# Optimization experiments

Hardware: AMD Instinct MI355X
Metric: run time of the kernel (lower is better)

The kernel has to match this reference:

```python
import jax, jax.numpy as jnp
import numpy as np

N_NODES = 100000
N_EDGES = 1600000
NODE_DIM = 128
EDGE_DIM = 32
HIDDEN = 64
OUT = 64


def setup_inputs() -> dict:
    key = jax.random.key(0)
    ks = jax.random.split(key, 16)
    s = lambda d: 1.0 / np.sqrt(d)
    inp = {
        'node_features': jax.random.normal(ks[0], (N_NODES, NODE_DIM), dtype=jnp.float32),
        'edge_indices': jax.random.randint(ks[1], (2, N_EDGES), 0, N_NODES, dtype=jnp.int64),
        'edge_features': jax.random.normal(ks[2], (N_EDGES, EDGE_DIM), dtype=jnp.float32),
        # node_transform / edge_transform
        'wn': jax.random.uniform(ks[3], (NODE_DIM, HIDDEN), jnp.float32, -s(NODE_DIM), s(NODE_DIM)),
        'bn': jax.random.uniform(ks[4], (HIDDEN,), jnp.float32, -s(NODE_DIM), s(NODE_DIM)),
        'we': jax.random.uniform(ks[5], (EDGE_DIM, HIDDEN), jnp.float32, -s(EDGE_DIM), s(EDGE_DIM)),
        'be': jax.random.uniform(ks[6], (HIDDEN,), jnp.float32, -s(EDGE_DIM), s(EDGE_DIM)),
        # message_mlp: Linear(2H,H) -> ReLU -> Linear(H,OUT)
        'wm1': jax.random.uniform(ks[7], (2 * HIDDEN, HIDDEN), jnp.float32, -s(2 * HIDDEN), s(2 * HIDDEN)),
        'bm1': jax.random.uniform(ks[8], (HIDDEN,), jnp.float32, -s(2 * HIDDEN), s(2 * HIDDEN)),
        'wm2': jax.random.uniform(ks[9], (HIDDEN, OUT), jnp.float32, -s(HIDDEN), s(HIDDEN)),
        'bm2': jax.random.uniform(ks[10], (OUT,), jnp.float32, -s(HIDDEN), s(HIDDEN)),
        # update_mlp: Linear(NODE_DIM+OUT,H) -> ReLU -> Linear(H,OUT)
        'wu1': jax.random.uniform(ks[11], (NODE_DIM + OUT, HIDDEN), jnp.float32, -s(NODE_DIM + OUT), s(NODE_DIM + OUT)),
        'bu1': jax.random.uniform(ks[12], (HIDDEN,), jnp.float32, -s(NODE_DIM + OUT), s(NODE_DIM + OUT)),
        'wu2': jax.random.uniform(ks[13], (HIDDEN, OUT), jnp.float32, -s(HIDDEN), s(HIDDEN)),
        'bu2': jax.random.uniform(ks[14], (OUT,), jnp.float32, -s(HIDDEN), s(HIDDEN)),
    }
    return inp


def reference(node_features, edge_indices, edge_features, wn, bn, we, be,
              wm1, bm1, wm2, bm2, wu1, bu1, wu2, bu2):
    node_emb = node_features @ wn + bn              # [N, H]
    edge_emb = edge_features @ we + be              # [E, H]
    src, dst = edge_indices[0], edge_indices[1]
    messages = jnp.concatenate([node_emb[src], edge_emb], axis=-1)  # [E, 2H]
    messages = jax.nn.relu(messages @ wm1 + bm1) @ wm2 + bm2        # [E, OUT]
    aggregated = jax.ops.segment_sum(messages, dst, num_segments=node_emb.shape[0])  # [N, OUT]
    updated = jnp.concatenate([node_features, aggregated], axis=-1)  # [N, NODE_DIM+OUT]
    return jax.nn.relu(updated @ wu1 + bu1) @ wu2 + bu2              # [N, OUT]
```

## Files before the change

kernel.cpp:

```cpp
#include <hip/hip_runtime.h>

#define NN 100000
#define NE 1600000

typedef __attribute__((ext_vector_type(8))) short bf16x8;
typedef __attribute__((ext_vector_type(4))) float f32x4;

#define OFF_M    0
#define OFF_B    (OFF_M + 16384)
#define OFF_C    (OFF_B + 2048)
#define OFF_W2U  (OFF_C + 64)
#define OFF_D2   (OFF_W2U + 4096)
#define OFF_BFRG (OFF_D2 + 64)
#define OFF_MFRG (OFF_BFRG + 1024)
#define OFF_W2UF (OFF_MFRG + 8192)
#define OFF_WU2F (OFF_W2UF + 2048)
#define OFF_BSUM (OFF_WU2F + 2048)
#define OFF_BOFF (OFF_BSUM + 128)
#define OFF_PRA  (OFF_BOFF + 128)
#define OFF_PRAH (OFF_PRA + NN * 64)
#define OFF_PRU  (OFF_PRAH + NN * 32)
#define OFF_H    (OFF_PRU + NN * 64)
#define OFF_HIST (OFF_H + NN * 64)
#define OFF_STRT (OFF_HIST + NN)
#define OFF_POS  (OFF_STRT + NN + 4)
#define OFF_HS   (OFF_POS + NE)
#define WS_UNITS (OFF_HS + NE * 32)

__device__ __forceinline__ unsigned bfr(float x) {
  unsigned u = __float_as_uint(x);
  return (u + 0x7fffu + ((u >> 16) & 1u)) >> 16;
}
__device__ __forceinline__ float bf2f(unsigned short h) {
  return __uint_as_float(((unsigned)h) << 16);
}
__device__ __forceinline__ unsigned addrelu1(unsigned qa, unsigned pb) {
  float lo = __uint_as_float((qa & 0xffffu) << 16) +
             __uint_as_float((pb & 0xffffu) << 16);
  float hi = __uint_as_float(qa & 0xffff0000u) +
             __uint_as_float(pb & 0xffff0000u);
  lo = fmaxf(lo, 0.f);
  hi = fmaxf(hi, 0.f);
  return bfr(lo) | (bfr(hi) << 16);
}
__device__ __forceinline__ uint4 addrelu4(uint4 q, uint4 p) {
  return make_uint4(addrelu1(q.x, p.x), addrelu1(q.y, p.y),
                    addrelu1(q.z, p.z), addrelu1(q.w, p.w));
}

__global__ __launch_bounds__(256) void k_fold(
    const float* __restrict__ wn, const float* __restrict__ bn,
    const float* __restrict__ we, const float* __restrict__ be,
    const float* __restrict__ wm1, const float* __restrict__ bm1,
    const float* __restrict__ wm2, const float* __restrict__ bm2,
    const float* __restrict__ wu1, const float* __restrict__ wu2,
    float* __restrict__ M, float* __restrict__ B, float* __restrict__ c,
    float* __restrict__ W2U, float* __restrict__ d2,
    uint4* __restrict__ Bfrag, uint4* __restrict__ Mfrag,
    uint4* __restrict__ W2Uf, uint4* __restrict__ wu2f) {
  int t = blockIdx.x * 256 + threadIdx.x;
  if (t < 16384) {
    int k = t >> 7, j = t & 127;
    float acc;
    if (j < 64) {
      acc = 0.f;
      for (int h = 0; h < 64; ++h) acc += wn[k * 64 + h] * wm1[h * 64 + j];
    } else {
      acc = wu1[k * 64 + (j - 64)];
    }
    M[t] = acc;
  } else if (t < 16384 + 2048) {
    int u = t - 16384;
    int k = u >> 6, j = u & 63;
    float acc = 0.f;
    for (int h = 0; h < 64; ++h) acc += we[k * 64 + h] * wm1[(64 + h) * 64 + j];
    B[u] = acc;
  } else if (t < 16384 + 2048 + 64) {
    int j = t - (16384 + 2048);
    float acc = bm1[j];
    for (int h = 0; h < 64; ++h)
      acc += bn[h] * wm1[h * 64 + j] + be[h] * wm1[(64 + h) * 64 + j];
    c[j] = acc;
  } else if (t < 16384 + 2048 + 64 + 4096) {
    int u = t - (16384 + 2048 + 64);
    int k = u >> 6, j = u & 63;
    float acc = 0.f;
    for (int h = 0; h < 64; ++h) acc += wm2[k * 64 + h] * wu1[(128 + h) * 64 + j];
    W2U[u] = acc;
  } else if (t < 16384 + 2048 + 64 + 4096 + 64) {
    int j = t - (16384 + 2048 + 64 + 4096);
    float acc = 0.f;
    for (int h = 0; h < 64; ++h) acc += bm2[h] * wu1[(128 + h) * 64 + j];
    d2[j] = acc;
  } else if (t < 16384 + 2048 + 64 + 4096 + 64 + 256) {
    int u = t - (16384 + 2048 + 64 + 4096 + 64);
    int jb = u >> 6, l = u & 63;
    int g = l >> 4, n = l & 15;
    unsigned s[8];
#pragma unroll
    for (int i = 0; i < 8; ++i) {
      int k = g * 8 + i;
      int j = jb * 16 + n;
      float acc = 0.f;
      for (int h = 0; h < 64; ++h)
        acc += we[k * 64 + h] * wm1[(64 + h) * 64 + j];
      s[i] = bfr(acc);
    }
    Bfrag[jb * 64 + l] = make_uint4(s[0] | (s[1] << 16), s[2] | (s[3] << 16),
                                    s[4] | (s[5] << 16), s[6] | (s[7] << 16));
  } else if (t < 16384 + 2048 + 64 + 4096 + 64 + 256 + 2048) {
    int u = t - (16384 + 2048 + 64 + 4096 + 64 + 256);
    int jb = u >> 8, kb = (u >> 6) & 3, l = u & 63;
    int g = l >> 4, n = l & 15;
    int j = jb * 16 + n;
    unsigned s[8];
#pragma unroll
    for (int i = 0; i < 8; ++i) {
      int k = kb * 32 + g * 8 + i;
      float acc;
      if (j < 64) {
        acc = 0.f;
        for (int h = 0; h < 64; ++h) acc += wn[k * 64 + h] * wm1[h * 64 + j];
      } else {
        acc = wu1[k * 64 + (j - 64)];
      }
      s[i] = bfr(acc);
    }
    Mfrag[(jb * 4 + kb) * 64 + l] =
        make_uint4(s[0] | (s[1] << 16), s[2] | (s[3] << 16),
                   s[4] | (s[5] << 16), s[6] | (s[7] << 16));
  } else if (t < 16384 + 2048 + 64 + 4096 + 64 + 256 + 2048 + 512) {
    int u = t - (16384 + 2048 + 64 + 4096 + 64 + 256 + 2048);
    int jk = u >> 6, l = u & 63;
    int jb = jk >> 1, kb = jk & 1;
    int g = l >> 4, n = l & 15;
    int j = jb * 16 + n;
    unsigned s[8];
#pragma unroll
    for (int i = 0; i < 8; ++i) {
      int k = kb * 32 + g * 8 + i;
      float acc = 0.f;
      for (int h = 0; h < 64; ++h)
        acc += wm2[k * 64 + h] * wu1[(128 + h) * 64 + j];
      s[i] = bfr(acc);
    }
    W2Uf[jk * 64 + l] = make_uint4(s[0] | (s[1] << 16), s[2] | (s[3] << 16),
                                   s[4] | (s[5] << 16), s[6] | (s[7] << 16));
  } else if (t < 16384 + 2048 + 64 + 4096 + 64 + 256 + 2048 + 512 + 512) {
    int u = t - (16384 + 2048 + 64 + 4096 + 64 + 256 + 2048 + 512);
    int jk = u >> 6, l = u & 63;
    int jb = jk >> 1, kb = jk & 1;
    int g = l >> 4, n = l & 15;
    unsigned s[8];
#pragma unroll
    for (int i = 0; i < 8; ++i)
      s[i] = bfr(wu2[(size_t)(kb * 32 + g * 8 + i) * 64 + jb * 16 + n]);
    wu2f[jk * 64 + l] = make_uint4(s[0] | (s[1] << 16), s[2] | (s[3] << 16),
                                   s[4] | (s[5] << 16), s[6] | (s[7] << 16));
  }
}

__global__ __launch_bounds__(256) void k_node2(
    const float* __restrict__ nf, const uint4* __restrict__ Mfrag,
    float* __restrict__ PRA, uint4* __restrict__ PRAh,
    float* __restrict__ PRU, int writePRA) {
  __shared__ unsigned short ldsP[4][16 * 72];
  int wib = threadIdx.x >> 6;
  int lane = threadIdx.x & 63;
  int tile = blockIdx.x * 4 + wib;
  if (tile >= NN / 16) return;
  int m = lane & 15, g = lane >> 4;
  int node = tile * 16 + m;

  bf16x8 a[4];
#pragma unroll
  for (int kb = 0; kb < 4; ++kb) {
    const float* __restrict__ rp = &nf[(size_t)node * 128 + kb * 32 + g * 8];
    float4 f0 = *(const float4*)rp;
    float4 f1 = *(const float4*)(rp + 4);
    bf16x8 v;
    v[0] = (short)bfr(f0.x); v[1] = (short)bfr(f0.y);
    v[2] = (short)bfr(f0.z); v[3] = (short)bfr(f0.w);
    v[4] = (short)bfr(f1.x); v[5] = (short)bfr(f1.y);
    v[6] = (short)bfr(f1.z); v[7] = (short)bfr(f1.w);
    a[kb] = v;
  }

  const bf16x8* __restrict__ mfp = (const bf16x8*)Mfrag;
  unsigned short* __restrict__ lp = &ldsP[wib][0];
#pragma unroll
  for (int jb = 0; jb < 8; ++jb) {
    f32x4 acc = {0.f, 0.f, 0.f, 0.f};
    acc = __builtin_amdgcn_mfma_f32_16x16x32_bf16(a[0], mfp[(jb * 4 + 0) * 64 + lane], acc, 0, 0, 0);
    acc = __builtin_amdgcn_mfma_f32_16x16x32_bf16(a[1], mfp[(jb * 4 + 1) * 64 + lane], acc, 0, 0, 0);
    acc = __builtin_amdgcn_mfma_f32_16x16x32_bf16(a[2], mfp[(jb * 4 + 2) * 64 + lane], acc, 0, 0, 0);
    acc = __builtin_amdgcn_mfma_f32_16x16x32_bf16(a[3], mfp[(jb * 4 + 3) * 64 + lane], acc, 0, 0, 0);
    int col = (jb & 3) * 16 + m;
    if (jb < 4) {
#pragma unroll
      for (int r = 0; r < 4; ++r)
        lp[(g * 4 + r) * 72 + col] = (unsigned short)bfr(acc[r]);
      if (writePRA) {
#pragma unroll
        for (int r = 0; r < 4; ++r)
          PRA[(size_t)(tile * 16 + g * 4 + r) * 64 + col] = acc[r];
      }
    } else {
#pragma unroll
      for (int r = 0; r < 4; ++r)
        PRU[(size_t)(tile * 16 + g * 4 + r) * 64 + col] = acc[r];
    }
  }
  __syncthreads();

  int m2 = lane >> 2, lo = lane & 3;
  uint4 w0 = *(const uint4*)&ldsP[wib][m2 * 72 + lo * 8];
  uint4 w1 = *(const uint4*)&ldsP[wib][m2 * 72 + 32 + lo * 8];
  uint4* __restrict__ pp = &PRAh[(size_t)(tile * 16 + m2) * 8];
  pp[lo] = w0;
  pp[4 + lo] = w1;
}

__global__ __launch_bounds__(256) void k_hist(const int* __restrict__ idx,
                                              int* __restrict__ hist,
                                              int* __restrict__ posOf) {
  int e = blockIdx.x * 256 + threadIdx.x;
  if (e < NE) posOf[e] = atomicAdd(&hist[idx[NE + e]], 1);
}

__global__ __launch_bounds__(1024) void k_scanA(const int* __restrict__ hist,
                                                int* __restrict__ strt,
                                                int* __restrict__ bsum) {
  __shared__ int lds[1024];
  int t = threadIdx.x;
  int i = blockIdx.x * 1024 + t;
  int v = (i < NN) ? hist[i] : 0;
  lds[t] = v;
  __syncthreads();
  for (int off = 1; off < 1024; off <<= 1) {
    int u = (t >= off) ? lds[t - off] : 0;
    __syncthreads();
    lds[t] += u;
    __syncthreads();
  }
  if (i < NN) strt[i] = lds[t] - v;
  if (t == 1023) bsum[blockIdx.x] = lds[1023];
}

__global__ __launch_bounds__(128) void k_scanB(const int* __restrict__ bsum,
                                               int* __restrict__ boff,
                                               int* __restrict__ strt,
                                               int nblocks) {
  __shared__ int lds[128];
  int t = threadIdx.x;
  int v = (t < nblocks) ? bsum[t] : 0;
  lds[t] = v;
  __syncthreads();
  for (int off = 1; off < 128; off <<= 1) {
    int u = (t >= off) ? lds[t - off] : 0;
    __syncthreads();
    lds[t] += u;
    __syncthreads();
  }
  if (t < nblocks) boff[t] = lds[t] - v;
  if (t == 127) strt[NN] = lds[127];
}

__global__ __launch_bounds__(1024) void k_scanC(int* __restrict__ strt,
                                                const int* __restrict__ boff) {
  int i = blockIdx.x * 1024 + threadIdx.x;
  if (i < NN) strt[i] += boff[blockIdx.x];
}

__global__ __launch_bounds__(256) void k_msgh(
    const int* __restrict__ idx, const int* __restrict__ strt,
    const int* __restrict__ posOf, const float* __restrict__ ef,
    const uint4* __restrict__ Bfrag, const float* __restrict__ c,
    const uint4* __restrict__ PRAh, unsigned short* __restrict__ hS) {
  __shared__ unsigned short ldsQ[4][16 * 72];
  int wib = threadIdx.x >> 6;
  int lane = threadIdx.x & 63;
  int m = lane & 15, g = lane >> 4;
  int tile = blockIdx.x * 4 + wib;

  int m2 = lane >> 2, lo = lane & 3;
  int e6 = tile * 16 + m2;
  int src6 = idx[e6];
  int dst6 = idx[NE + e6];
  int pos6 = posOf[e6];
  uint4 p0 = PRAh[(size_t)src6 * 8 + lo];
  uint4 p1 = PRAh[(size_t)src6 * 8 + 4 + lo];
  int slot = strt[dst6] + pos6;

  const float* __restrict__ rp = &ef[(size_t)(tile * 16 + m) * 32 + g * 8];
  float4 f0 = *(const float4*)rp;
  float4 f1 = *(const float4*)(rp + 4);
  bf16x8 a;
  a[0] = (short)bfr(f0.x); a[1] = (short)bfr(f0.y);
  a[2] = (short)bfr(f0.z); a[3] = (short)bfr(f0.w);
  a[4] = (short)bfr(f1.x); a[5] = (short)bfr(f1.y);
  a[6] = (short)bfr(f1.z); a[7] = (short)bfr(f1.w);

  const bf16x8* __restrict__ bfp = (const bf16x8*)Bfrag;
  bf16x8 b0 = bfp[0 * 64 + lane];
  bf16x8 b1 = bfp[1 * 64 + lane];
  bf16x8 b2 = bfp[2 * 64 + lane];
  bf16x8 b3 = bfp[3 * 64 + lane];
  float cl0 = c[0 * 16 + m], cl1 = c[1 * 16 + m];
  float cl2 = c[2 * 16 + m], cl3 = c[3 * 16 + m];

  f32x4 z = {0.f, 0.f, 0.f, 0.f};
  f32x4 q0 = __builtin_amdgcn_mfma_f32_16x16x32_bf16(a, b0, z, 0, 0, 0);
  f32x4 q1 = __builtin_amdgcn_mfma_f32_16x16x32_bf16(a, b1, z, 0, 0, 0);
  f32x4 q2 = __builtin_amdgcn_mfma_f32_16x16x32_bf16(a, b2, z, 0, 0, 0);
  f32x4 q3 = __builtin_amdgcn_mfma_f32_16x16x32_bf16(a, b3, z, 0, 0, 0);

  unsigned short* __restrict__ lq = &ldsQ[wib][0];
#pragma unroll
  for (int r = 0; r < 4; ++r) {
    int mp = g * 4 + r;
    lq[mp * 72 + 0 * 16 + m] = (unsigned short)bfr(q0[r] + cl0);
    lq[mp * 72 + 1 * 16 + m] = (unsigned short)bfr(q1[r] + cl1);
    lq[mp * 72 + 2 * 16 + m] = (unsigned short)bfr(q2[r] + cl2);
    lq[mp * 72 + 3 * 16 + m] = (unsigned short)bfr(q3[r] + cl3);
  }
  __syncthreads();

  uint4 w0 = *(const uint4*)&ldsQ[wib][m2 * 72 + lo * 8];
  uint4 w1 = *(const uint4*)&ldsQ[wib][m2 * 72 + 32 + lo * 8];
  uint4 h0 = addrelu4(w0, p0);
  uint4 h1 = addrelu4(w1, p1);
  uint4* __restrict__ qp = (uint4*)(hS + (size_t)slot * 64);
  qp[lo] = h0;
  qp[4 + lo] = h1;
}

__global__ __launch_bounds__(256) void k_sum(
    const unsigned short* __restrict__ hS, const int* __restrict__ strt,
    unsigned* __restrict__ Hb) {
  int wib = threadIdx.x >> 6;
  int lane = threadIdx.x & 63;
  int n = blockIdx.x * 4 + wib;
  if (n >= NN) return;
  int s0 = strt[n], s1 = strt[n + 1];
  float acc = 0.f;
  int s = s0;
  for (; s + 4 <= s1; s += 4) {
    unsigned short a0 = hS[(size_t)(s + 0) * 64 + lane];
    unsigned short a1 = hS[(size_t)(s + 1) * 64 + lane];
    unsigned short a2 = hS[(size_t)(s + 2) * 64 + lane];
    unsigned short a3 = hS[(size_t)(s + 3) * 64 + lane];
    acc += (bf2f(a0) + bf2f(a1)) + (bf2f(a2) + bf2f(a3));
  }
  for (; s < s1; ++s) acc += bf2f(hS[(size_t)s * 64 + lane]);
  float other = __shfl_xor(acc, 1);
  if ((lane & 1) == 0)
    Hb[(size_t)n * 32 + (lane >> 1)] = bfr(acc) | (bfr(other) << 16);
}

__global__ __launch_bounds__(256) void k_update5(
    const unsigned* __restrict__ Hb, const int* __restrict__ strt,
    const float* __restrict__ PRU,
    const uint4* __restrict__ W2Uf, const float* __restrict__ d2,
    const float* __restrict__ bu1,
    const uint4* __restrict__ wu2f, const float* __restrict__ bu2,
    float* __restrict__ out) {
  __shared__ unsigned short ldsH[4][16 * 72];
  int wib = threadIdx.x >> 6;
  int lane = threadIdx.x & 63;
  int tile = blockIdx.x * 4 + wib;
  if (tile >= NN / 16) return;
  int m = lane & 15, g = lane >> 4;
  int node = tile * 16 + m;

  bf16x8 ah[2];
  ah[0] = *(const bf16x8*)&Hb[(size_t)node * 32 + 0 * 16 + g * 4];
  ah[1] = *(const bf16x8*)&Hb[(size_t)node * 32 + 1 * 16 + g * 4];

  float deg[4];
#pragma unroll
  for (int r = 0; r < 4; ++r) {
    int row = tile * 16 + g * 4 + r;
    deg[r] = (float)(strt[row + 1] - strt[row]);
  }

  const bf16x8* __restrict__ w2p = (const bf16x8*)W2Uf;
  const bf16x8* __restrict__ wup = (const bf16x8*)wu2f;
  unsigned short* __restrict__ lh = &ldsH[wib][0];

#pragma unroll
  for (int jb = 0; jb < 4; ++jb) {
    f32x4 acc = {0.f, 0.f, 0.f, 0.f};
    acc = __builtin_amdgcn_mfma_f32_16x16x32_bf16(ah[0], w2p[(jb * 2 + 0) * 64 + lane], acc, 0, 0, 0);
    acc = __builtin_amdgcn_mfma_f32_16x16x32_bf16(ah[1], w2p[(jb * 2 + 1) * 64 + lane], acc, 0, 0, 0);
    int col = jb * 16 + m;
    float dc = d2[col], bc = bu1[col];
#pragma unroll
    for (int r = 0; r < 4; ++r) {
      int row = tile * 16 + g * 4 + r;
      float pre = acc[r] + PRU[(size_t)row * 64 + col] + deg[r] * dc + bc;
      lh[(g * 4 + r) * 72 + col] = (unsigned short)bfr(fmaxf(pre, 0.f));
    }
  }
  __syncthreads();

  bf16x8 a2[2];
  a2[0] = *(const bf16x8*)&lh[m * 72 + 0 * 32 + g * 8];
  a2[1] = *(const bf16x8*)&lh[m * 72 + 1 * 32 + g * 8];
#pragma unroll
  for (int jb = 0; jb < 4; ++jb) {
    f32x4 acc = {0.f, 0.f, 0.f, 0.f};
    acc = __builtin_amdgcn_mfma_f32_16x16x32_bf16(a2[0], wup[(jb * 2 + 0) * 64 + lane], acc, 0, 0, 0);
    acc = __builtin_amdgcn_mfma_f32_16x16x32_bf16(a2[1], wup[(jb * 2 + 1) * 64 + lane], acc, 0, 0, 0);
    int col = jb * 16 + m;
    float bc = bu2[col];
#pragma unroll
    for (int r = 0; r < 4; ++r) {
      int row = tile * 16 + g * 4 + r;
      out[(size_t)row * 64 + col] = acc[r] + bc;
    }
  }
}

__global__ __launch_bounds__(256) void k_edge_at(
    const int* __restrict__ idx, const float* __restrict__ ef,
    const float* __restrict__ B, const float* __restrict__ c,
    const float* __restrict__ wm2, const float* __restrict__ bm2,
    const float* __restrict__ PRA, float* __restrict__ agg) {
  int e = blockIdx.x * 256 + threadIdx.x;
  if (e >= NE) return;
  int src = idx[e];
  int dst = idx[NE + e];
  float efr[32];
#pragma unroll
  for (int k = 0; k < 32; k += 4)
    *(float4*)&efr[k] = *(const float4*)&ef[(size_t)e * 32 + k];
  float m[64];
#pragma unroll
  for (int o = 0; o < 64; ++o) m[o] = bm2[o];
  const float* __restrict__ prs = &PRA[(size_t)src * 64];
#pragma unroll 1
  for (int jc = 0; jc < 64; jc += 16) {
    float q[16];
#pragma unroll
    for (int jj = 0; jj < 16; ++jj) q[jj] = c[jc + jj];
#pragma unroll
    for (int k = 0; k < 32; ++k) {
      float ev = efr[k];
#pragma unroll
      for (int jj = 0; jj < 16; ++jj) q[jj] += ev * B[k * 64 + jc + jj];
    }
#pragma unroll
    for (int jj = 0; jj < 16; ++jj) {
      float h = fmaxf(prs[jc + jj] + q[jj], 0.f);
#pragma unroll
      for (int o = 0; o < 64; ++o) m[o] += h * wm2[(jc + jj) * 64 + o];
    }
  }
  float* __restrict__ ap = &agg[(size_t)dst * 64];
#pragma unroll
  for (int o = 0; o < 64; ++o) atomicAdd(&ap[o], m[o]);
}

__global__ __launch_bounds__(256) void k_update_at(
    const float* __restrict__ agg, const float* __restrict__ PRU,
    const float* __restrict__ wu1, const float* __restrict__ bu1,
    const float* __restrict__ wu2, const float* __restrict__ bu2,
    float* __restrict__ out) {
  int n = blockIdx.x * 256 + threadIdx.x;
  if (n >= NN) return;
  float ar[64];
#pragma unroll
  for (int k = 0; k < 64; k += 4)
    *(float4*)&ar[k] = *(const float4*)&agg[(size_t)n * 64 + k];
  float acc[64];
#pragma unroll
  for (int o = 0; o < 64; ++o) acc[o] = bu2[o];
  const float* __restrict__ prs = &PRU[(size_t)n * 64];
#pragma unroll 1
  for (int jc = 0; jc < 64; jc += 16) {
    float q[16];
#pragma unroll
    for (int jj = 0; jj < 16; ++jj) q[jj] = bu1[jc + jj];
#pragma unroll
    for (int k = 0; k < 64; ++k) {
      float av = ar[k];
#pragma unroll
      for (int jj = 0; jj < 16; ++jj) q[jj] += av * wu1[(128 + k) * 64 + jc + jj];
    }
#pragma unroll
    for (int jj = 0; jj < 16; ++jj) {
      float h = fmaxf(prs[jc + jj] + q[jj], 0.f);
#pragma unroll
      for (int o = 0; o < 64; ++o) acc[o] += h * wu2[(jc + jj) * 64 + o];
    }
  }
#pragma unroll
  for (int o = 0; o < 64; o += 4)
    *(float4*)&out[(size_t)n * 64 + o] = make_float4(acc[o], acc[o + 1], acc[o + 2], acc[o + 3]);
}

extern "C" void kernel_launch(void* const* d_in, const int* in_sizes, int n_in,
                              void* d_out, int out_size, void* d_ws, size_t ws_size,
                              hipStream_t stream) {
  const float* nf  = (const float*)d_in[0];
  const int*   idx = (const int*)d_in[1];
  const float* ef  = (const float*)d_in[2];
  const float* wn  = (const float*)d_in[3];
  const float* bn  = (const float*)d_in[4];
  const float* we  = (const float*)d_in[5];
  const float* be  = (const float*)d_in[6];
  const float* wm1 = (const float*)d_in[7];
  const float* bm1 = (const float*)d_in[8];
  const float* wm2 = (const float*)d_in[9];
  const float* bm2 = (const float*)d_in[10];
  const float* wu1 = (const float*)d_in[11];
  const float* bu1 = (const float*)d_in[12];
  const float* wu2 = (const float*)d_in[13];
  const float* bu2 = (const float*)d_in[14];
  float* out = (float*)d_out;

  float* ws   = (float*)d_ws;
  float* M    = ws + OFF_M;
  float* B    = ws + OFF_B;
  float* c    = ws + OFF_C;
  float* W2U  = ws + OFF_W2U;
  float* d2   = ws + OFF_D2;
  uint4* Bfrg = (uint4*)(ws + OFF_BFRG);
  uint4* Mfrg = (uint4*)(ws + OFF_MFRG);
  uint4* W2Uf = (uint4*)(ws + OFF_W2UF);
  uint4* wu2f = (uint4*)(ws + OFF_WU2F);
  int*   bsum = (int*)(ws + OFF_BSUM);
  int*   boff = (int*)(ws + OFF_BOFF);
  float* PRA  = ws + OFF_PRA;
  uint4* PRAh = (uint4*)(ws + OFF_PRAH);
  float* PRU  = ws + OFF_PRU;
  float* H    = ws + OFF_H;
  unsigned* Hb = (unsigned*)(ws + OFF_H);
  int*   hist = (int*)(ws + OFF_HIST);
  int*   strt = (int*)(ws + OFF_STRT);
  int*   posOf = (int*)(ws + OFF_POS);
  unsigned short* hS = (unsigned short*)(ws + OFF_HS);

  const int SCAN_BLOCKS = (NN + 1023) / 1024;
  const int FOLD_THREADS = 16384 + 2048 + 64 + 4096 + 64 + 256 + 2048 + 512 + 512;
  const int NTILE = NN / 16;

  int fast = (ws_size >= (size_t)WS_UNITS * 4);

  k_fold<<<(FOLD_THREADS + 255) / 256, 256, 0, stream>>>(
      wn, bn, we, be, wm1, bm1, wm2, bm2, wu1, wu2,
      M, B, c, W2U, d2, Bfrg, Mfrg, W2Uf, wu2f);
  k_node2<<<(NTILE + 3) / 4, 256, 0, stream>>>(nf, Mfrg, PRA, PRAh, PRU,
                                               fast ? 0 : 1);

  if (fast) {
    hipMemsetAsync(hist, 0, (size_t)NN * sizeof(int), stream);
    k_hist<<<(NE + 255) / 256, 256, 0, stream>>>(idx, hist, posOf);
    k_scanA<<<SCAN_BLOCKS, 1024, 0, stream>>>(hist, strt, bsum);
    k_scanB<<<1, 128, 0, stream>>>(bsum, boff, strt, SCAN_BLOCKS);
    k_scanC<<<SCAN_BLOCKS, 1024, 0, stream>>>(strt, boff);
    k_msgh<<<NE / 16 / 4, 256, 0, stream>>>(idx, strt, posOf, ef, Bfrg, c,
                                            PRAh, hS);
    k_sum<<<(NN + 3) / 4, 256, 0, stream>>>(hS, strt, Hb);
    k_update5<<<(NTILE + 3) / 4, 256, 0, stream>>>(
        Hb, strt, PRU, W2Uf, d2, bu1, wu2f, bu2, out);
  } else {
    hipMemsetAsync(H, 0, (size_t)NN * 64 * sizeof(float), stream);
    k_edge_at<<<(NE + 255) / 256, 256, 0, stream>>>(idx, ef, B, c, wm2, bm2, PRA, H);
    k_update_at<<<(NN + 255) / 256, 256, 0, stream>>>(
        H, PRU, wu1, bu1, wu2, bu2, out);
  }
}
```

Baseline: 340.7 us.

## Fuse segment-sum into update kernel, staging aggregates in LDS

Merges the per-node segment-sum kernel into the update MLP kernel. Each wave sums the sorted message rows for its 16 nodes, writes packed bf16 aggregates to shared memory, and feeds them straight into the MFMA update. This drops one launch and the global round trip of the aggregate buffer. In exchange each wave now walks 16 nodes one after another, so fewer waves run the gather at once, which can cut latency hiding and memory-level parallelism.

```diff
diff --git a/kernel.cpp b/kernel.cpp
--- a/kernel.cpp
+++ b/kernel.cpp
@@ -335,47 +335,46 @@
   qp[4 + lo] = h1;
 }
 
-__global__ __launch_bounds__(256) void k_sum(
+__global__ __launch_bounds__(256) void k_sumup(
     const unsigned short* __restrict__ hS, const int* __restrict__ strt,
-    unsigned* __restrict__ Hb) {
-  int wib = threadIdx.x >> 6;
-  int lane = threadIdx.x & 63;
-  int n = blockIdx.x * 4 + wib;
-  if (n >= NN) return;
-  int s0 = strt[n], s1 = strt[n + 1];
-  float acc = 0.f;
-  int s = s0;
-  for (; s + 4 <= s1; s += 4) {
-    unsigned short a0 = hS[(size_t)(s + 0) * 64 + lane];
-    unsigned short a1 = hS[(size_t)(s + 1) * 64 + lane];
-    unsigned short a2 = hS[(size_t)(s + 2) * 64 + lane];
-    unsigned short a3 = hS[(size_t)(s + 3) * 64 + lane];
-    acc += (bf2f(a0) + bf2f(a1)) + (bf2f(a2) + bf2f(a3));
-  }
-  for (; s < s1; ++s) acc += bf2f(hS[(size_t)s * 64 + lane]);
-  float other = __shfl_xor(acc, 1);
-  if ((lane & 1) == 0)
-    Hb[(size_t)n * 32 + (lane >> 1)] = bfr(acc) | (bfr(other) << 16);
-}
-
-__global__ __launch_bounds__(256) void k_update5(
-    const unsigned* __restrict__ Hb, const int* __restrict__ strt,
     const float* __restrict__ PRU,
     const uint4* __restrict__ W2Uf, const float* __restrict__ d2,
     const float* __restrict__ bu1,
     const uint4* __restrict__ wu2f, const float* __restrict__ bu2,
     float* __restrict__ out) {
+  __shared__ unsigned ldsHb[4][16 * 36];
   __shared__ unsigned short ldsH[4][16 * 72];
   int wib = threadIdx.x >> 6;
   int lane = threadIdx.x & 63;
   int tile = blockIdx.x * 4 + wib;
   if (tile >= NN / 16) return;
   int m = lane & 15, g = lane >> 4;
-  int node = tile * 16 + m;
+
+  unsigned* __restrict__ hb = &ldsHb[wib][0];
+
+#pragma unroll 1
+  for (int i = 0; i < 16; ++i) {
+    int row = tile * 16 + i;
+    int s0 = strt[row], s1 = strt[row + 1];
+    float acc = 0.f;
+    int s = s0;
+    for (; s + 4 <= s1; s += 4) {
+      unsigned short a0 = hS[(size_t)(s + 0) * 64 + lane];
+      unsigned short a1 = hS[(size_t)(s + 1) * 64 + lane];
+      unsigned short a2 = hS[(size_t)(s + 2) * 64 + lane];
+      unsigned short a3 = hS[(size_t)(s + 3) * 64 + lane];
+      acc += (bf2f(a0) + bf2f(a1)) + (bf2f(a2) + bf2f(a3));
+    }
+    for (; s < s1; ++s) acc += bf2f(hS[(size_t)s * 64 + lane]);
+    float other = __shfl_xor(acc, 1);
+    if ((lane & 1) == 0)
+      hb[i * 36 + (lane >> 1)] = bfr(acc) | (bfr(other) << 16);
+  }
+  __syncthreads();
 
   bf16x8 ah[2];
-  ah[0] = *(const bf16x8*)&Hb[(size_t)node * 32 + 0 * 16 + g * 4];
-  ah[1] = *(const bf16x8*)&Hb[(size_t)node * 32 + 1 * 16 + g * 4];
+  ah[0] = *(const bf16x8*)&hb[m * 36 + 0 * 16 + g * 4];
+  ah[1] = *(const bf16x8*)&hb[m * 36 + 1 * 16 + g * 4];
 
   float deg[4];
 #pragma unroll
@@ -536,7 +535,6 @@
   uint4* PRAh = (uint4*)(ws + OFF_PRAH);
   float* PRU  = ws + OFF_PRU;
   float* H    = ws + OFF_H;
-  unsigned* Hb = (unsigned*)(ws + OFF_H);
   int*   hist = (int*)(ws + OFF_HIST);
   int*   strt = (int*)(ws + OFF_STRT);
   int*   posOf = (int*)(ws + OFF_POS);
@@ -562,9 +560,8 @@
     k_scanC<<<SCAN_BLOCKS, 1024, 0, stream>>>(strt, boff);
     k_msgh<<<NE / 16 / 4, 256, 0, stream>>>(idx, strt, posOf, ef, Bfrg, c,
                                             PRAh, hS);
-    k_sum<<<(NN + 3) / 4, 256, 0, stream>>>(hS, strt, Hb);
-    k_update5<<<(NTILE + 3) / 4, 256, 0, stream>>>(
-        Hb, strt, PRU, W2Uf, d2, bu1, wu2f, bu2, out);
+    k_sumup<<<(NTILE + 3) / 4, 256, 0, stream>>>(
+        hS, strt, PRU, W2Uf, d2, bu1, wu2f, bu2, out);
   } else {
     hipMemsetAsync(H, 0, (size_t)NN * 64 * sizeof(float), stream);
     k_edge_at<<<(NE + 255) / 256, 256, 0, stream>>>(idx, ef, B, c, wm2, bm2, PRA, H);
```

Result: no change. 345.5 us (+1.4%).
